# Kernel tuning notes

Measured on AMD Instinct MI355X. Metric: run time of the kernel, lower is better.

The kernel has to match this reference:

```python
import jax, jax.numpy as jnp
import numpy as np

N_NODES = 100000
N_EDGES = 1600000
N_GRAPHS = 512
IN_DIM = 64
HID = 64
OUT_DIM = 2


def setup_inputs() -> dict:
    key = jax.random.key(0)
    ks = jax.random.split(key, 8)
    x = jax.random.normal(ks[0], (N_NODES, IN_DIM), dtype=jnp.float32)
    edge_index = jax.random.randint(ks[1], (2, N_EDGES), 0, N_NODES, dtype=jnp.int64)
    batch = jnp.sort(jax.random.randint(ks[2], (N_NODES,), 0, N_GRAPHS, dtype=jnp.int64))
    s1 = 1.0 / np.sqrt(IN_DIM)
    s2 = 1.0 / np.sqrt(HID)
    W1 = jax.random.normal(ks[3], (IN_DIM, HID), dtype=jnp.float32) * s1
    b1 = jnp.zeros((HID,), dtype=jnp.float32)
    W2 = jax.random.normal(ks[4], (HID, HID), dtype=jnp.float32) * s2
    b2 = jnp.zeros((HID,), dtype=jnp.float32)
    Wfc = jax.random.normal(ks[5], (HID, OUT_DIM), dtype=jnp.float32) * s2
    bfc = jnp.zeros((OUT_DIM,), dtype=jnp.float32)
    return {"x": x, "edge_index": edge_index, "batch": batch,
            "W1": W1, "b1": b1, "W2": W2, "b2": b2, "Wfc": Wfc, "bfc": bfc}


def _gcn_conv(x, src, dst, dinv, W, b):
    # PyG GCNConv: h = D^{-1/2}(A+I)D^{-1/2} X W + b, self-loops already in src/dst
    h = x @ W  # [N, H]
    norm = dinv[src] * dinv[dst]  # [E+N]
    msg = h[src] * norm[:, None]  # gather over edges
    return jax.ops.segment_sum(msg, dst, num_segments=N_NODES) + b


def reference(x, edge_index, batch, W1, b1, W2, b2, Wfc, bfc):
    loops = jnp.arange(N_NODES, dtype=edge_index.dtype)
    src = jnp.concatenate([edge_index[0], loops])
    dst = jnp.concatenate([edge_index[1], loops])
    deg = jax.ops.segment_sum(jnp.ones_like(dst, dtype=x.dtype), dst, num_segments=N_NODES)
    dinv = jnp.where(deg > 0, jax.lax.rsqrt(jnp.maximum(deg, 1.0)), 0.0)
    h = jax.nn.relu(_gcn_conv(x, src, dst, dinv, W1, b1))
    h = jax.nn.relu(_gcn_conv(h, src, dst, dinv, W2, b2))
    # global mean pool over graphs
    sums = jax.ops.segment_sum(h, batch, num_segments=N_GRAPHS)
    cnts = jax.ops.segment_sum(jnp.ones((N_NODES,), dtype=h.dtype), batch, num_segments=N_GRAPHS)
    pooled = sums / jnp.maximum(cnts, 1.0)[:, None]
    return pooled @ Wfc + bfc
```

## Files before the change

kernel.cpp:

```cpp
#include <hip/hip_runtime.h>
#include <hip/hip_fp16.h>

#define NN 100000
#define NE 1600000
#define NG 512
#define FD 64
#define NSL 4
#define CHUNK 128
#define SCAN_CHUNK 1024
#define SCAN_BLOCKS 98

union U32H2 { unsigned u; __half2 h; };
__device__ inline __half2 h2(unsigned v) { U32H2 c; c.u = v; return c.h; }
__device__ inline unsigned uh(__half2 v) { U32H2 c; c.h = v; return c.u; }
__device__ inline unsigned pack_f16x2(float a, float b) {
    return uh(__floats2half2_rn(a, b));
}


__global__ void k_count_rank(const int* __restrict__ dst, int* __restrict__ cnt,
                             int* __restrict__ rank, int e) {
    int i = blockIdx.x * 256 + threadIdx.x;
    if (i < e) rank[i] = atomicAdd(&cnt[dst[i]], 1);
}

__global__ void k_scan1(const int* __restrict__ cnt, int* __restrict__ part,
                        int* __restrict__ blockSum, int n) {
    __shared__ int lds[256];
    int tid = threadIdx.x;
    int base = blockIdx.x * SCAN_CHUNK + tid * 4;
    int v0 = (base + 0 < n) ? cnt[base + 0] : 0;
    int v1 = (base + 1 < n) ? cnt[base + 1] : 0;
    int v2 = (base + 2 < n) ? cnt[base + 2] : 0;
    int v3 = (base + 3 < n) ? cnt[base + 3] : 0;
    int s = v0 + v1 + v2 + v3;
    lds[tid] = s;
    __syncthreads();
    for (int off = 1; off < 256; off <<= 1) {
        int t = (tid >= off) ? lds[tid - off] : 0;
        __syncthreads();
        lds[tid] += t;
        __syncthreads();
    }
    int run = lds[tid] - s;
    if (base + 0 < n) part[base + 0] = run; run += v0;
    if (base + 1 < n) part[base + 1] = run; run += v1;
    if (base + 2 < n) part[base + 2] = run; run += v2;
    if (base + 3 < n) part[base + 3] = run;
    if (tid == 255) blockSum[blockIdx.x] = lds[255];
}

__global__ void k_scan2(const int* __restrict__ bs, int* __restrict__ boff, int nb) {
    __shared__ int lds[128];
    int tid = threadIdx.x;
    int v = (tid < nb) ? bs[tid] : 0;
    lds[tid] = v;
    __syncthreads();
    for (int off = 1; off < 128; off <<= 1) {
        int t = (tid >= off) ? lds[tid - off] : 0;
        __syncthreads();
        lds[tid] += t;
        __syncthreads();
    }
    if (tid < nb) boff[tid] = lds[tid] - v;
}

__global__ void k_scan3(int* __restrict__ rowptr, const int* __restrict__ boff,
                        const int* __restrict__ cnt, float* __restrict__ dinv, int n) {
    int i = blockIdx.x * 256 + threadIdx.x;
    if (i < n) {
        rowptr[i] = rowptr[i] + boff[i >> 10];
        float deg = (float)(cnt[i] + 1);
        dinv[i] = 1.0f / sqrtf(deg);
    }
}

__global__ void k_pcnt_bs(const int* __restrict__ batch, int* __restrict__ pcnt, int n, int ng) {
    int g = blockIdx.x * 256 + threadIdx.x;
    if (g >= ng) return;
    int lo = 0, hi = n;
    while (lo < hi) { int m = (lo + hi) >> 1; if (batch[m] < g) lo = m + 1; else hi = m; }
    int l0 = lo;
    lo = 0; hi = n;
    int v = g + 1;
    while (lo < hi) { int m = (lo + hi) >> 1; if (batch[m] < v) lo = m + 1; else hi = m; }
    pcnt[g] = lo - l0;
}

__global__ void k_fill(const int* __restrict__ src, const int* __restrict__ dst,
                       const int* __restrict__ rank, const int* __restrict__ rowptr,
                       int* __restrict__ colidx, int e) {
    int i = blockIdx.x * 256 + threadIdx.x;
    if (i < e) {
        int d = dst[i];
        colidx[rowptr[d] + rank[i]] = src[i];
    }
}

template <int F16IN>
__global__ void k_gemm_scale(const void* __restrict__ inv_, const float* __restrict__ W,
                             const float* __restrict__ dinv, unsigned* __restrict__ hs, int n) {
    __shared__ float w[FD * FD];
    __shared__ float xr[4][4][80];
    int tid = threadIdx.x;
    {
        const float4* W4 = (const float4*)W;
        float4* w4s = (float4*)w;
        for (int i = tid; i < FD * FD / 4; i += 256) w4s[i] = W4[i];
    }
    int wave = tid >> 6, lane = tid & 63;
    int r = lane >> 4;
    int c = lane & 15;
    int row = blockIdx.x * 16 + wave * 4 + r;
    bool valid = row < n;
    if (valid) {
        if (F16IN) {
            uint2 v = ((const uint2*)inv_)[((size_t)(c >> 2) * NN + row) * 4 + (c & 3)];
            float2 f0 = __half22float2(h2(v.x));
            float2 f1 = __half22float2(h2(v.y));
            xr[wave][r][c * 4 + 0] = f0.x;
            xr[wave][r][c * 4 + 1] = f0.y;
            xr[wave][r][c * 4 + 2] = f1.x;
            xr[wave][r][c * 4 + 3] = f1.y;
        } else {
            float4 xv = ((const float4*)inv_)[row * 16 + c];
            *((float4*)&xr[wave][r][c * 4]) = xv;
        }
    }
    __syncthreads();
    if (!valid) return;
    const float4* w4 = (const float4*)w;
    float4 acc = {0.f, 0.f, 0.f, 0.f};
#pragma unroll
    for (int k = 0; k < FD; ++k) {
        float xv = xr[wave][r][k];
        float4 wv = w4[k * 16 + c];
        acc.x = fmaf(xv, wv.x, acc.x);
        acc.y = fmaf(xv, wv.y, acc.y);
        acc.z = fmaf(xv, wv.z, acc.z);
        acc.w = fmaf(xv, wv.w, acc.w);
    }
    float d = dinv[row];
    uint2 o;
    o.x = pack_f16x2(acc.x * d, acc.y * d);
    o.y = pack_f16x2(acc.z * d, acc.w * d);
    ((uint2*)hs)[((size_t)(c >> 2) * NN + row) * 4 + (c & 3)] = o;
}

template <int POOL>
__global__ void k_agg4(const unsigned* __restrict__ hs, const int* __restrict__ rowptr,
                       const int* __restrict__ cnt, const int* __restrict__ colidx,
                       const float* __restrict__ dinv, const float* __restrict__ b,
                       const int* __restrict__ batch, void* __restrict__ outp, int n) {
    int bid = blockIdx.x;
    int s = bid & 3;
    int chunk = bid >> 2;
    int tid = threadIdx.x;
    int wave = tid >> 6, lane = tid & 63;
    int slot = lane >> 3, fp = lane & 7;
    const unsigned* S = hs + (size_t)s * NN * 8;
    float b0 = b[s * 16 + fp * 2], b1 = b[s * 16 + fp * 2 + 1];
    int node = chunk * CHUNK + wave;
    if (node >= n) return;
    int rs = rowptr[node], ct = cnt[node];
    float dv = dinv[node];
    int bg = POOL ? batch[node] : 0;
    int c0 = colidx[rs + slot];
    int c1 = colidx[rs + 8 + slot];
    int curg = bg;
    float p0 = 0.f, p1 = 0.f;
    for (int t = 0; t < CHUNK / 4; ++t) {
        bool ok0 = slot < ct, ok1 = slot + 8 < ct;
        int i0 = ok0 ? c0 : node;
        int i1 = ok1 ? c1 : node;
        unsigned w0 = S[(size_t)i0 * 8 + fp];
        unsigned w1 = S[(size_t)i1 * 8 + fp];
        unsigned sv = S[(size_t)node * 8 + fp];
        int node2 = node + 4;
        int ncl = node2 < n ? node2 : n - 1;
        int rs2 = rowptr[ncl], ct2 = cnt[ncl];
        float dv2 = dinv[ncl];
        int bg2 = POOL ? batch[ncl] : 0;
        int nc0 = colidx[rs2 + slot];
        int nc1 = colidx[rs2 + 8 + slot];
        w0 = ok0 ? w0 : 0u;
        w1 = ok1 ? w1 : 0u;
        __half2 acc = __hadd2(h2(w0), h2(w1));
        int e = rs + ct;
        for (int i = rs + 16; i < e; i += 8) {
            int cc = colidx[i + slot];
            bool ok = (i + slot) < e;
            int ii = ok ? cc : node;
            unsigned ww = S[(size_t)ii * 8 + fp];
            ww = ok ? ww : 0u;
            acc = __hadd2(acc, h2(ww));
        }
        acc = __hadd2(acc, h2(__shfl_xor(uh(acc), 8, 64)));
        acc = __hadd2(acc, h2(__shfl_xor(uh(acc), 16, 64)));
        acc = __hadd2(acc, h2(__shfl_xor(uh(acc), 32, 64)));
        float2 av = __half22float2(acc);
        float2 sf = __half22float2(h2(sv));
        float r0 = fmaxf(fmaf(av.x + sf.x, dv, b0), 0.f);
        float r1 = fmaxf(fmaf(av.y + sf.y, dv, b1), 0.f);
        if (POOL) {
            if (bg != curg) {
                if (lane < 8) {
                    float* p = &((float*)outp)[((size_t)s * NG + curg) * 16 + fp * 2];
                    atomicAdd(p + 0, p0);
                    atomicAdd(p + 1, p1);
                }
                curg = bg; p0 = 0.f; p1 = 0.f;
            }
            p0 += r0; p1 += r1;
        } else if (lane < 8) {
            ((unsigned*)outp)[((size_t)s * NN + node) * 8 + fp] = pack_f16x2(r0, r1);
        }
        node = node2;
        if (node >= n) break;
        rs = rs2; ct = ct2; dv = dv2; bg = bg2; c0 = nc0; c1 = nc1;
    }
    if (POOL && lane < 8) {
        float* p = &((float*)outp)[((size_t)s * NG + curg) * 16 + fp * 2];
        atomicAdd(p + 0, p0);
        atomicAdd(p + 1, p1);
    }
}

__global__ void k_final(const float* __restrict__ pool, const int* __restrict__ pcnt,
                        const float* __restrict__ Wfc, const float* __restrict__ bfc,
                        float* __restrict__ out, int ng) {
    int tid = threadIdx.x;
    int wave = tid >> 6, lane = tid & 63;
    int g = blockIdx.x * 4 + wave;
    if (g >= ng) return;
    float inv = 1.0f / fmaxf((float)pcnt[g], 1.0f);
    float s = pool[((size_t)(lane >> 4) * NG + g) * 16 + (lane & 15)] * inv;
    float a0 = s * Wfc[lane * 2 + 0];
    float a1 = s * Wfc[lane * 2 + 1];
#pragma unroll
    for (int off = 32; off > 0; off >>= 1) {
        a0 += __shfl_down(a0, off, 64);
        a1 += __shfl_down(a1, off, 64);
    }
    if (lane == 0) {
        out[g * 2 + 0] = a0 + bfc[0];
        out[g * 2 + 1] = a1 + bfc[1];
    }
}

extern "C" void kernel_launch(void* const* d_in, const int* in_sizes, int n_in,
                              void* d_out, int out_size, void* d_ws, size_t ws_size,
                              hipStream_t stream) {
    const float* x    = (const float*)d_in[0];
    const int*   eidx = (const int*)d_in[1];
    const int*   batch= (const int*)d_in[2];
    const float* W1   = (const float*)d_in[3];
    const float* b1   = (const float*)d_in[4];
    const float* W2   = (const float*)d_in[5];
    const float* b2   = (const float*)d_in[6];
    const float* Wfc  = (const float*)d_in[7];
    const float* bfc  = (const float*)d_in[8];
    float* out = (float*)d_out;

    const int* esrc = eidx;
    const int* edst = eidx + NE;

    char* ws = (char*)d_ws;
    size_t off = 0;
    auto alloc = [&](size_t bytes) {
        char* p = ws + off;
        off += (bytes + 255) & ~(size_t)255;
        return p;
    };
    int*      cnt      = (int*)     alloc(NN * 4);
    int*      rowptr   = (int*)     alloc(NN * 4);
    int*      blockSum = (int*)     alloc(128 * 4);
    int*      blockOff = (int*)     alloc(128 * 4);
    float*    dinv     = (float*)   alloc(NN * 4);
    int*      colidx   = (int*)     alloc((size_t)(NE + 64) * 4);
    unsigned* hs       = (unsigned*)alloc((size_t)NN * FD * 2);
    unsigned* h1       = (unsigned*)alloc((size_t)NN * FD * 2);
    float*    pool     = (float*)   alloc((size_t)NSL * NG * 16 * 4);
    int*      pcnt     = (int*)     alloc(NG * 4);
    int*      rank     = (int*)h1;
    (void)ws_size;

    hipMemsetAsync(cnt,  0, NN * 4, stream);
    hipMemsetAsync(pool, 0, (size_t)NSL * NG * 16 * 4, stream);

    const int GE = (NE + 255) / 256;
    const int GN = (NN + 255) / 256;
    const int GR = (NN + 15) / 16;
    const int GA = ((NN + CHUNK - 1) / CHUNK) * NSL;

    k_count_rank<<<GE, 256, 0, stream>>>(edst, cnt, rank, NE);
    k_scan1<<<SCAN_BLOCKS, 256, 0, stream>>>(cnt, rowptr, blockSum, NN);
    k_scan2<<<1, 128, 0, stream>>>(blockSum, blockOff, SCAN_BLOCKS);
    k_scan3<<<GN, 256, 0, stream>>>(rowptr, blockOff, cnt, dinv, NN);
    k_pcnt_bs<<<2, 256, 0, stream>>>(batch, pcnt, NN, NG);
    k_fill<<<GE, 256, 0, stream>>>(esrc, edst, rank, rowptr, colidx, NE);

    k_gemm_scale<0><<<GR, 256, 0, stream>>>(x, W1, dinv, hs, NN);
    k_agg4<0><<<GA, 256, 0, stream>>>(hs, rowptr, cnt, colidx, dinv, b1, batch, h1, NN);

    k_gemm_scale<1><<<GR, 256, 0, stream>>>(h1, W2, dinv, hs, NN);
    k_agg4<1><<<GA, 256, 0, stream>>>(hs, rowptr, cnt, colidx, dinv, b2, batch, pool, NN);

    k_final<<<(NG + 3) / 4, 256, 0, stream>>>(pool, pcnt, Wfc, bfc, out, NG);
}
```

Baseline: 373.9 us.

## Deepen software pipeline in GCN aggregation to prefetch gathers one node ahead

Restructures the per-wave node loop into a three-stage pipeline. Row metadata is loaded three nodes ahead, column indices two ahead, and the feature gathers for the next node are issued before the current node is reduced. It also widens the unrolled gather from 16 to 32 neighbours when the degree exceeds 16. The aim is to hide gather latency on this memory-bound sparse aggregation, at the cost of more registers and redundant clamped work for the tail nodes.

```diff
diff --git a/kernel.cpp b/kernel.cpp
--- a/kernel.cpp
+++ b/kernel.cpp
@@ -147,6 +147,32 @@
     ((uint2*)hs)[((size_t)(c >> 2) * NN + row) * 4 + (c & 3)] = o;
 }
 
+struct G5 { unsigned w0, w1, w2, w3, sv; };
+__device__ inline G5 issue_gather(const unsigned* __restrict__ S,
+                                  int c0, int c1, int c2, int c3,
+                                  int ct, int nc, int slot, int fp) {
+    G5 g;
+    bool o0 = slot < ct, o1 = slot + 8 < ct;
+    int i0 = o0 ? c0 : nc;
+    int i1 = o1 ? c1 : nc;
+    unsigned t0 = S[(size_t)i0 * 8 + fp];
+    unsigned t1 = S[(size_t)i1 * 8 + fp];
+    g.sv = S[(size_t)nc * 8 + fp];
+    g.w0 = o0 ? t0 : 0u;
+    g.w1 = o1 ? t1 : 0u;
+    g.w2 = 0u; g.w3 = 0u;
+    if (ct > 16) {
+        bool o2 = slot + 16 < ct, o3 = slot + 24 < ct;
+        int i2 = o2 ? c2 : nc;
+        int i3 = o3 ? c3 : nc;
+        unsigned t2 = S[(size_t)i2 * 8 + fp];
+        unsigned t3 = S[(size_t)i3 * 8 + fp];
+        g.w2 = o2 ? t2 : 0u;
+        g.w3 = o3 ? t3 : 0u;
+    }
+    return g;
+}
+
 template <int POOL>
 __global__ void k_agg4(const unsigned* __restrict__ hs, const int* __restrict__ rowptr,
                        const int* __restrict__ cnt, const int* __restrict__ colidx,
@@ -160,64 +186,85 @@
     int slot = lane >> 3, fp = lane & 7;
     const unsigned* S = hs + (size_t)s * NN * 8;
     float b0 = b[s * 16 + fp * 2], b1 = b[s * 16 + fp * 2 + 1];
-    int node = chunk * CHUNK + wave;
-    if (node >= n) return;
-    int rs = rowptr[node], ct = cnt[node];
-    float dv = dinv[node];
-    int bg = POOL ? batch[node] : 0;
-    int c0 = colidx[rs + slot];
-    int c1 = colidx[rs + 8 + slot];
-    int curg = bg;
+
+    int base = chunk * CHUNK + wave;
+    auto cl = [n](int i) { return i < n ? i : n - 1; };
+
+    int nA = cl(base);
+    int rsA = rowptr[nA], ctA = cnt[nA];
+    float dvA = dinv[nA];
+    int bgA = POOL ? batch[nA] : 0;
+    int nB = cl(base + 4);
+    int rsB = rowptr[nB], ctB = cnt[nB];
+    float dvB = dinv[nB];
+    int bgB = POOL ? batch[nB] : 0;
+    int nC = cl(base + 8);
+    int rsC = rowptr[nC], ctC = cnt[nC];
+    float dvC = dinv[nC];
+    int bgC = POOL ? batch[nC] : 0;
+
+    int cA0 = colidx[rsA + slot];
+    int cA1 = colidx[rsA + 8 + slot];
+    int cA2 = 0, cA3 = 0;
+    if (ctA > 16) { cA2 = colidx[rsA + 16 + slot]; cA3 = colidx[rsA + 24 + slot]; }
+    int cB0 = colidx[rsB + slot];
+    int cB1 = colidx[rsB + 8 + slot];
+    int cB2 = 0, cB3 = 0;
+    if (ctB > 16) { cB2 = colidx[rsB + 16 + slot]; cB3 = colidx[rsB + 24 + slot]; }
+
+    G5 g = issue_gather(S, cA0, cA1, cA2, cA3, ctA, nA, slot, fp);
+
+    int curg = bgA;
     float p0 = 0.f, p1 = 0.f;
+
     for (int t = 0; t < CHUNK / 4; ++t) {
-        bool ok0 = slot < ct, ok1 = slot + 8 < ct;
-        int i0 = ok0 ? c0 : node;
-        int i1 = ok1 ? c1 : node;
-        unsigned w0 = S[(size_t)i0 * 8 + fp];
-        unsigned w1 = S[(size_t)i1 * 8 + fp];
-        unsigned sv = S[(size_t)node * 8 + fp];
-        int node2 = node + 4;
-        int ncl = node2 < n ? node2 : n - 1;
-        int rs2 = rowptr[ncl], ct2 = cnt[ncl];
-        float dv2 = dinv[ncl];
-        int bg2 = POOL ? batch[ncl] : 0;
-        int nc0 = colidx[rs2 + slot];
-        int nc1 = colidx[rs2 + 8 + slot];
-        w0 = ok0 ? w0 : 0u;
-        w1 = ok1 ? w1 : 0u;
-        __half2 acc = __hadd2(h2(w0), h2(w1));
-        int e = rs + ct;
-        for (int i = rs + 16; i < e; i += 8) {
-            int cc = colidx[i + slot];
-            bool ok = (i + slot) < e;
-            int ii = ok ? cc : node;
-            unsigned ww = S[(size_t)ii * 8 + fp];
-            ww = ok ? ww : 0u;
-            acc = __hadd2(acc, h2(ww));
+        int nt = base + t * 4;
+        G5 gn = issue_gather(S, cB0, cB1, cB2, cB3, ctB, cl(nt + 4), slot, fp);
+        int n3 = cl(nt + 12);
+        int rsD = rowptr[n3], ctD = cnt[n3];
+        float dvD = dinv[n3];
+        int bgD = POOL ? batch[n3] : 0;
+        int cC0 = colidx[rsC + slot];
+        int cC1 = colidx[rsC + 8 + slot];
+        int cC2 = 0, cC3 = 0;
+        if (ctC > 16) { cC2 = colidx[rsC + 16 + slot]; cC3 = colidx[rsC + 24 + slot]; }
+        __half2 acc = __hadd2(__hadd2(h2(g.w0), h2(g.w1)), __hadd2(h2(g.w2), h2(g.w3)));
+        if (ctA > 32) {
+            int nc = cl(nt);
+            int e = rsA + ctA;
+            for (int i = rsA + 32; i < e; i += 8) {
+                int cc = colidx[i + slot];
+                bool ok = (i + slot) < e;
+                int ii = ok ? cc : nc;
+                unsigned ww = S[(size_t)ii * 8 + fp];
+                acc = __hadd2(acc, h2(ok ? ww : 0u));
+            }
         }
         acc = __hadd2(acc, h2(__shfl_xor(uh(acc), 8, 64)));
         acc = __hadd2(acc, h2(__shfl_xor(uh(acc), 16, 64)));
         acc = __hadd2(acc, h2(__shfl_xor(uh(acc), 32, 64)));
         float2 av = __half22float2(acc);
-        float2 sf = __half22float2(h2(sv));
-        float r0 = fmaxf(fmaf(av.x + sf.x, dv, b0), 0.f);
-        float r1 = fmaxf(fmaf(av.y + sf.y, dv, b1), 0.f);
+        float2 sf = __half22float2(h2(g.sv));
+        float r0 = fmaxf(fmaf(av.x + sf.x, dvA, b0), 0.f);
+        float r1 = fmaxf(fmaf(av.y + sf.y, dvA, b1), 0.f);
         if (POOL) {
-            if (bg != curg) {
+            if (bgA != curg) {
                 if (lane < 8) {
                     float* p = &((float*)outp)[((size_t)s * NG + curg) * 16 + fp * 2];
                     atomicAdd(p + 0, p0);
                     atomicAdd(p + 1, p1);
                 }
-                curg = bg; p0 = 0.f; p1 = 0.f;
+                curg = bgA; p0 = 0.f; p1 = 0.f;
             }
-            p0 += r0; p1 += r1;
-        } else if (lane < 8) {
-            ((unsigned*)outp)[((size_t)s * NN + node) * 8 + fp] = pack_f16x2(r0, r1);
+            if (nt < n) { p0 += r0; p1 += r1; }
+        } else if (lane < 8 && nt < n) {
+            ((unsigned*)outp)[((size_t)s * NN + nt) * 8 + fp] = pack_f16x2(r0, r1);
         }
-        node = node2;
-        if (node >= n) break;
-        rs = rs2; ct = ct2; dv = dv2; bg = bg2; c0 = nc0; c1 = nc1;
+        rsA = rsB; ctA = ctB; dvA = dvB; bgA = bgB;
+        rsB = rsC; ctB = ctC; dvB = dvC; bgB = bgC;
+        rsC = rsD; ctC = ctD; dvC = dvD; bgC = bgD;
+        cB0 = cC0; cB1 = cC1; cB2 = cC2; cB3 = cC3;
+        g = gn;
     }
     if (POOL && lane < 8) {
         float* p = &((float*)outp)[((size_t)s * NG + curg) * 16 + fp * 2];
```

New measurement: 363.0 us. 1.03x faster.
